# Kernel tuning notes

Hardware: AMD Instinct MI355X
Metric: run time of the kernel (lower is better)

## Reference

```python
import jax, jax.numpy as jnp
import numpy as np

N, E, HID, STRUCT = 50000, 800000, 128, 7
GAMMA, DELTA = 1.0, 0.5
LN_EPS = 1e-5


def seg_softmax(score, seg, num_segments):
    m = jax.ops.segment_max(score, seg, num_segments=num_segments)
    e = jnp.exp(score - m[seg])
    s = jax.ops.segment_sum(e, seg, num_segments=num_segments)
    return e / s[seg]


def setup_inputs() -> dict:
    key = jax.random.key(0)
    ks = jax.random.split(key, 16)
    w = lambda k, shp: (jax.random.normal(k, shp, dtype=jnp.float32) * 0.1)
    return {
        "edge_index": jax.random.randint(ks[0], (2, E), 0, N, dtype=jnp.int32),
        "h": jax.random.normal(ks[1], (N, HID), dtype=jnp.float32),
        "W_att": w(ks[2], (HID, HID)),
        "phi_att_w": w(ks[3], (HID, HID)),
        "phi_att_b": jnp.zeros((HID,), jnp.float32),
        "W_p": w(ks[4], (HID, HID)),
        "W_p_prime": w(ks[5], (HID, HID)),
        "f_def_w": w(ks[6], (HID, 1)),
        "f_def_b": jnp.zeros((1,), jnp.float32),
        "W_self_w": w(ks[7], (HID, HID)),
        "W_self_b": jnp.zeros((HID,), jnp.float32),
        "W_A_w": w(ks[8], (HID, HID)),
        "W_A_b": jnp.zeros((HID,), jnp.float32),
        "W_str_w": w(ks[9], (STRUCT - 1, HID)),
        "W_str_b": jnp.zeros((HID,), jnp.float32),
        "ln_g": jnp.ones((HID,), jnp.float32),
        "ln_b": jnp.zeros((HID,), jnp.float32),
    }


def reference(edge_index, h, W_att, phi_att_w, phi_att_b, W_p, W_p_prime,
              f_def_w, f_def_b, W_self_w, W_self_b, W_A_w, W_A_b,
              W_str_w, W_str_b, ln_g, ln_b):
    H = h  # in_dim == hidden_dim -> embed is None
    s_feat = h[:, : STRUCT - 1]                       # [N, 6]
    src, tgt = edge_index[0], edge_index[1]
    h_src, h_tgt = H[src], H[tgt]                     # [E, HID]
    s_src, s_tgt = s_feat[src], s_feat[tgt]           # [E, 6]

    # attention scores, scatter-softmax over tgt
    W_hs = h_src @ W_att
    score = jnp.sum(h_tgt * W_hs, -1) + jnp.sum(s_src * s_tgt, -1)
    alpha = seg_softmax(score, tgt, N)                # [E]

    # defense term on reversed edges: rev_src = tgt, rev_tgt = src
    h_att, h_def = H[src], H[tgt]                     # H[rev_tgt], H[rev_src]
    pair = jnp.sum((h_att @ W_p) * (h_def @ W_p_prime), -1)
    beta = seg_softmax(pair, src, N)                  # softmax over rev_tgt = src
    psi = (h_def @ f_def_w + f_def_b)[:, 0]           # [E]
    sum_term = jax.ops.segment_sum(beta * jnp.exp(-psi), src, num_segments=N)
    d = -jnp.log(sum_term + 1e-8)
    rho = jax.nn.sigmoid(GAMMA * (d - DELTA))         # [N]

    rho_edge = rho[src]
    m_e = alpha[:, None] * (h_src @ phi_att_w + phi_att_b) * (1.0 - rho_edge)[:, None]
    m_att = jax.ops.segment_sum(m_e, tgt, num_segments=N)  # [N, HID]

    H_new = jax.nn.relu(H @ W_self_w + W_self_b + m_att @ W_A_w + W_A_b
                        + s_feat @ W_str_w + W_str_b) + H
    mu = jnp.mean(H_new, -1, keepdims=True)
    var = jnp.mean((H_new - mu) ** 2, -1, keepdims=True)
    return (H_new - mu) * jax.lax.rsqrt(var + LN_EPS) * ln_g + ln_b
```

## Files before the change

kernel.cpp:

```cpp
#include <hip/hip_runtime.h>
#include <math.h>

#define HID 128
#define NSTR 6
#define GAMMA 1.0f
#define DELTA 0.5f
#define LN_EPS 1e-5f
#define KPAD 72
#define CSR_CHUNK 8192

typedef __attribute__((ext_vector_type(4))) float f4;
typedef __attribute__((ext_vector_type(8))) short bf16x8;
typedef __attribute__((ext_vector_type(4))) float f32x4;

__device__ __forceinline__ unsigned short f2bf(float f) {
    unsigned u = __float_as_uint(f);
    unsigned r = u + 0x7FFFu + ((u >> 16) & 1u);
    return (unsigned short)(r >> 16);
}
__device__ __forceinline__ float bf2f(unsigned short h) {
    return __uint_as_float((unsigned)h << 16);
}
__device__ __forceinline__ void split2(float v, unsigned short& h, unsigned short& l) {
    h = f2bf(v);
    l = f2bf(v - bf2f(h));
}
__device__ __forceinline__ void bf2f2(unsigned u, float& lo, float& hi) {
    lo = __uint_as_float(u << 16);
    hi = __uint_as_float(u & 0xFFFF0000u);
}
__device__ __forceinline__ void unpack8(const uint4 u, float* f) {
    bf2f2(u.x, f[0], f[1]); bf2f2(u.y, f[2], f[3]);
    bf2f2(u.z, f[4], f[5]); bf2f2(u.w, f[6], f[7]);
}

__global__ __launch_bounds__(256) void k_prep_all(
    const float* __restrict__ W_att, const float* __restrict__ Wself,
    const float* __restrict__ Wp,    const float* __restrict__ Wpp,
    const float* __restrict__ phiw,  const float* __restrict__ WA,
    const float* __restrict__ phib,
    unsigned short* __restrict__ WT, float* __restrict__ pbA)
{
    __shared__ float Bs[128][129];
    __shared__ float As[16][129];
    const int mode = blockIdx.y, c0 = blockIdx.x * 16;
    const int tid = threadIdx.x;
    const size_t MSZ = (size_t)2 * HID * HID;
    unsigned short* hi = WT + (size_t)mode * MSZ;
    unsigned short* lo = hi + HID * HID;

    if (mode == 0) {
        for (int idx = tid; idx < 2048; idx += 256) {
            const int c = idx >> 7, k = idx & 127;
            unsigned short h, l;
            split2(W_att[(size_t)(c0 + c) * HID + k], h, l);
            hi[(size_t)(c0 + c) * HID + k] = h;
            lo[(size_t)(c0 + c) * HID + k] = l;
        }
    } else if (mode == 1) {
        for (int idx = tid; idx < 2048; idx += 256) {
            const int k = idx >> 4, c = idx & 15;
            Bs[k][c] = Wself[k * HID + c0 + c];
        }
        __syncthreads();
        for (int idx = tid; idx < 2048; idx += 256) {
            const int c = idx >> 7, k = idx & 127;
            unsigned short h, l;
            split2(Bs[k][c], h, l);
            hi[(size_t)(c0 + c) * HID + k] = h;
            lo[(size_t)(c0 + c) * HID + k] = l;
        }
    } else if (mode == 2) {
        for (int idx = tid; idx < 128 * 128; idx += 256)
            Bs[idx >> 7][idx & 127] = Wpp[idx];
        for (int idx = tid; idx < 16 * 128; idx += 256)
            As[idx >> 7][idx & 127] = Wp[(size_t)(c0 + (idx >> 7)) * HID + (idx & 127)];
        __syncthreads();
        for (int it = 0; it < 8; ++it) {
            const int idx = tid + 256 * it;
            const int c = idx >> 7, k = idx & 127;
            float a = 0.f;
            #pragma unroll 4
            for (int j = 0; j < 128; ++j)
                a = fmaf(As[c][j], Bs[k][j], a);
            unsigned short h, l;
            split2(a, h, l);
            hi[(size_t)(c0 + c) * HID + k] = h;
            lo[(size_t)(c0 + c) * HID + k] = l;
        }
    } else {
        for (int idx = tid; idx < 128 * 128; idx += 256)
            Bs[idx >> 7][idx & 127] = phiw[idx];
        for (int idx = tid; idx < 16 * 128; idx += 256) {
            const int c = idx >> 7, j = idx & 127;
            As[c][j] = WA[(size_t)j * HID + c0 + c];
        }
        __syncthreads();
        for (int it = 0; it < 8; ++it) {
            const int idx = tid + 256 * it;
            const int c = idx >> 7, k = idx & 127;
            float a = 0.f;
            #pragma unroll 4
            for (int j = 0; j < 128; ++j)
                a = fmaf(As[c][j], Bs[k][j], a);
            unsigned short h, l;
            split2(a, h, l);
            hi[(size_t)(c0 + c) * HID + k] = h;
            lo[(size_t)(c0 + c) * HID + k] = l;
        }
        if (tid < 16) {
            float a = 0.f;
            #pragma unroll 4
            for (int j = 0; j < 128; ++j)
                a = fmaf(phib[j], As[tid][j], a);
            pbA[c0 + tid] = a;
        }
    }
}

__global__ __launch_bounds__(256) void k_castpsi(
    const float* __restrict__ H, const float* __restrict__ fw,
    const float* __restrict__ fb,
    unsigned short* __restrict__ HB, float* __restrict__ psi, int N)
{
    const int tid = threadIdx.x;
    const int row = blockIdx.x * 16 + (tid >> 4), sub = tid & 15;
    if (row >= N) return;
    const size_t o = (size_t)row * HID + sub * 8;
    const f4 v0 = *(const f4*)&H[o];
    const f4 v1 = *(const f4*)&H[o + 4];
    ushort4 a, b;
    a.x = f2bf(v0[0]); a.y = f2bf(v0[1]); a.z = f2bf(v0[2]); a.w = f2bf(v0[3]);
    b.x = f2bf(v1[0]); b.y = f2bf(v1[1]); b.z = f2bf(v1[2]); b.w = f2bf(v1[3]);
    *(ushort4*)&HB[o] = a;
    *(ushort4*)&HB[o + 4] = b;
    const f4 w0 = *(const f4*)&fw[sub * 8];
    const f4 w1 = *(const f4*)&fw[sub * 8 + 4];
    float s = v0[0]*w0[0] + v0[1]*w0[1] + v0[2]*w0[2] + v0[3]*w0[3]
            + v1[0]*w1[0] + v1[1]*w1[1] + v1[2]*w1[2] + v1[3]*w1[3];
    #pragma unroll
    for (int mk = 1; mk < 16; mk <<= 1) s += __shfl_xor(s, mk);
    if (sub == 0) psi[row] = s + fb[0];
}

struct GemmArgsT {
    const unsigned short* Whi[2];
    const unsigned short* Wlo[2];
    void*                 O[2];
    int                   of32[2];
};

__global__ __launch_bounds__(256, 2) void k_gemm(const float* __restrict__ A,
                                                 GemmArgsT g, int N)
{
    extern __shared__ unsigned short lds[];
    unsigned short* Ahi = lds;
    unsigned short* Alo = lds + 128 * KPAD;
    unsigned short* Bhi = lds + 2 * 128 * KPAD;
    unsigned short* Blo = lds + 3 * 128 * KPAD;
    const int tid  = threadIdx.x;
    const int row0 = blockIdx.x * 128;
    const int nrows = min(128, N - row0);
    const int ph   = blockIdx.y;
    const int w    = tid >> 6, lane = tid & 63;
    const int lrow = lane & 15, kgrp = lane >> 4;

    f32x4 acc[2][8];
    #pragma unroll
    for (int tc = 0; tc < 8; ++tc) {
        acc[0][tc] = f32x4{0.f, 0.f, 0.f, 0.f};
        acc[1][tc] = f32x4{0.f, 0.f, 0.f, 0.f};
    }

    const unsigned short* __restrict__ Wh = g.Whi[ph];
    const unsigned short* __restrict__ Wl = g.Wlo[ph];

    for (int ch = 0; ch < 2; ++ch) {
        __syncthreads();
        #pragma unroll
        for (int it = 0; it < 8; ++it) {
            const int idx = tid + 256 * it;
            const int r = idx >> 4, kq = (idx & 15) * 4;
            f4 v = {0.f, 0.f, 0.f, 0.f};
            if (r < nrows) v = *(const f4*)&A[(size_t)(row0 + r) * HID + ch * 64 + kq];
            ushort4 h, l;
            split2(v[0], h.x, l.x); split2(v[1], h.y, l.y);
            split2(v[2], h.z, l.z); split2(v[3], h.w, l.w);
            *(ushort4*)&Ahi[r * KPAD + kq] = h;
            *(ushort4*)&Alo[r * KPAD + kq] = l;
        }
        #pragma unroll
        for (int it = 0; it < 4; ++it) {
            const int idx = tid + 256 * it;
            const int c = idx >> 3, k8 = (idx & 7) * 8;
            *(uint4*)&Bhi[c * KPAD + k8] = *(const uint4*)&Wh[(size_t)c * HID + ch * 64 + k8];
            *(uint4*)&Blo[c * KPAD + k8] = *(const uint4*)&Wl[(size_t)c * HID + ch * 64 + k8];
        }
        __syncthreads();

        #pragma unroll
        for (int ks = 0; ks < 2; ++ks) {
            const int ko = ks * 32 + kgrp * 8;
            bf16x8 ah[2], al[2], bh[8], bl[8];
            #pragma unroll
            for (int tr = 0; tr < 2; ++tr) {
                const int rr = w * 32 + tr * 16 + lrow;
                ah[tr] = *(const bf16x8*)&Ahi[rr * KPAD + ko];
                al[tr] = *(const bf16x8*)&Alo[rr * KPAD + ko];
            }
            #pragma unroll
            for (int tc = 0; tc < 8; ++tc) {
                const int cc = tc * 16 + lrow;
                bh[tc] = *(const bf16x8*)&Bhi[cc * KPAD + ko];
                bl[tc] = *(const bf16x8*)&Blo[cc * KPAD + ko];
            }
            #pragma unroll
            for (int tr = 0; tr < 2; ++tr)
                #pragma unroll
                for (int tc = 0; tc < 8; ++tc) {
                    acc[tr][tc] = __builtin_amdgcn_mfma_f32_16x16x32_bf16(ah[tr], bh[tc], acc[tr][tc], 0, 0, 0);
                    acc[tr][tc] = __builtin_amdgcn_mfma_f32_16x16x32_bf16(al[tr], bh[tc], acc[tr][tc], 0, 0, 0);
                    acc[tr][tc] = __builtin_amdgcn_mfma_f32_16x16x32_bf16(ah[tr], bl[tc], acc[tr][tc], 0, 0, 0);
                }
        }
    }

    #pragma unroll
    for (int tr = 0; tr < 2; ++tr)
        #pragma unroll
        for (int j = 0; j < 4; ++j) {
            const int r = w * 32 + tr * 16 + kgrp * 4 + j;
            if (r < nrows) {
                if (g.of32[ph]) {
                    float* O = (float*)g.O[ph];
                    #pragma unroll
                    for (int tc = 0; tc < 8; ++tc)
                        O[(size_t)(row0 + r) * HID + tc * 16 + lrow] = acc[tr][tc][j];
                } else {
                    unsigned short* O = (unsigned short*)g.O[ph];
                    #pragma unroll
                    for (int tc = 0; tc < 8; ++tc)
                        O[(size_t)(row0 + r) * HID + tc * 16 + lrow] = f2bf(acc[tr][tc][j]);
                }
            }
        }
}

__global__ __launch_bounds__(256, 2) void k_final(
    const float* __restrict__ Agg, const float* __restrict__ H,
    const float* __restrict__ sig, const float* __restrict__ pbA,
    const unsigned short* __restrict__ Ghi, const unsigned short* __restrict__ Glo,
    const unsigned short* __restrict__ WShi, const unsigned short* __restrict__ WSlo,
    const float* __restrict__ Wstr,
    const float* __restrict__ bself, const float* __restrict__ bA,
    const float* __restrict__ bstr,
    const float* __restrict__ lng, const float* __restrict__ lnb,
    float* __restrict__ out, int N)
{
    extern __shared__ unsigned short lds[];
    unsigned short* Ahi = lds;
    unsigned short* Alo = lds + 128 * KPAD;
    unsigned short* Bhi = lds + 2 * 128 * KPAD;
    unsigned short* Blo = lds + 3 * 128 * KPAD;
    const int tid  = threadIdx.x;
    const int row0 = blockIdx.x * 128;
    const int nrows = min(128, N - row0);
    const int w    = tid >> 6, lane = tid & 63;
    const int lrow = lane & 15, kgrp = lane >> 4;

    f32x4 acc[2][8];
    float gl[8], bl_[8], pb[8];
    #pragma unroll
    for (int tc = 0; tc < 8; ++tc) {
        const int c = tc * 16 + lrow;
        const float bv = bself[c] + bA[c] + bstr[c];
        acc[0][tc] = f32x4{bv, bv, bv, bv};
        acc[1][tc] = f32x4{bv, bv, bv, bv};
        gl[tc] = lng[c]; bl_[tc] = lnb[c]; pb[tc] = pbA[c];
    }

    for (int ph = 0; ph < 2; ++ph) {
        const float* __restrict__ Am = ph ? H : Agg;
        const unsigned short* __restrict__ Wh = ph ? WShi : Ghi;
        const unsigned short* __restrict__ Wl = ph ? WSlo : Glo;
        for (int ch = 0; ch < 2; ++ch) {
            __syncthreads();
            #pragma unroll
            for (int it = 0; it < 8; ++it) {
                const int idx = tid + 256 * it;
                const int r = idx >> 4, kq = (idx & 15) * 4;
                f4 v = {0.f, 0.f, 0.f, 0.f};
                if (r < nrows) v = *(const f4*)&Am[(size_t)(row0 + r) * HID + ch * 64 + kq];
                ushort4 h, l;
                split2(v[0], h.x, l.x); split2(v[1], h.y, l.y);
                split2(v[2], h.z, l.z); split2(v[3], h.w, l.w);
                *(ushort4*)&Ahi[r * KPAD + kq] = h;
                *(ushort4*)&Alo[r * KPAD + kq] = l;
            }
            #pragma unroll
            for (int it = 0; it < 4; ++it) {
                const int idx = tid + 256 * it;
                const int c = idx >> 3, k8 = (idx & 7) * 8;
                *(uint4*)&Bhi[c * KPAD + k8] = *(const uint4*)&Wh[(size_t)c * HID + ch * 64 + k8];
                *(uint4*)&Blo[c * KPAD + k8] = *(const uint4*)&Wl[(size_t)c * HID + ch * 64 + k8];
            }
            __syncthreads();

            #pragma unroll
            for (int ks = 0; ks < 2; ++ks) {
                const int ko = ks * 32 + kgrp * 8;
                bf16x8 ah[2], al[2], bh[8], bl[8];
                #pragma unroll
                for (int tr = 0; tr < 2; ++tr) {
                    const int rr = w * 32 + tr * 16 + lrow;
                    ah[tr] = *(const bf16x8*)&Ahi[rr * KPAD + ko];
                    al[tr] = *(const bf16x8*)&Alo[rr * KPAD + ko];
                }
                #pragma unroll
                for (int tc = 0; tc < 8; ++tc) {
                    const int cc = tc * 16 + lrow;
                    bh[tc] = *(const bf16x8*)&Bhi[cc * KPAD + ko];
                    bl[tc] = *(const bf16x8*)&Blo[cc * KPAD + ko];
                }
                #pragma unroll
                for (int tr = 0; tr < 2; ++tr)
                    #pragma unroll
                    for (int tc = 0; tc < 8; ++tc) {
                        acc[tr][tc] = __builtin_amdgcn_mfma_f32_16x16x32_bf16(ah[tr], bh[tc], acc[tr][tc], 0, 0, 0);
                        acc[tr][tc] = __builtin_amdgcn_mfma_f32_16x16x32_bf16(al[tr], bh[tc], acc[tr][tc], 0, 0, 0);
                        acc[tr][tc] = __builtin_amdgcn_mfma_f32_16x16x32_bf16(ah[tr], bl[tc], acc[tr][tc], 0, 0, 0);
                    }
            }

            if (ph == 1 && ch == 0) {
                #pragma unroll
                for (int tr = 0; tr < 2; ++tr)
                    #pragma unroll
                    for (int j = 0; j < 4; ++j) {
                        const int rr = w * 32 + tr * 16 + kgrp * 4 + j;
                        float s[NSTR];
                        #pragma unroll
                        for (int k = 0; k < NSTR; ++k)
                            s[k] = bf2f(Ahi[rr * KPAD + k]) + bf2f(Alo[rr * KPAD + k]);
                        #pragma unroll
                        for (int tc = 0; tc < 8; ++tc) {
                            float a = 0.f;
                            #pragma unroll
                            for (int k = 0; k < NSTR; ++k)
                                a = fmaf(s[k], Wstr[k * HID + tc * 16 + lrow], a);
                            acc[tr][tc][j] += a;
                        }
                    }
            }
        }
    }

    #pragma unroll
    for (int tr = 0; tr < 2; ++tr)
        #pragma unroll
        for (int j = 0; j < 4; ++j) {
            const int r = w * 32 + tr * 16 + kgrp * 4 + j;
            const bool valid = r < nrows;
            const size_t rb = (size_t)(row0 + r) * HID;
            const float sg = valid ? sig[row0 + r] : 0.f;
            float v[8], s1 = 0.f, s2 = 0.f;
            #pragma unroll
            for (int tc = 0; tc < 8; ++tc) {
                float x = fmaxf(acc[tr][tc][j] + sg * pb[tc], 0.f);
                if (valid) x += H[rb + tc * 16 + lrow];
                v[tc] = x;
                s1 += x; s2 += x * x;
            }
            #pragma unroll
            for (int mk = 1; mk < 16; mk <<= 1) {
                s1 += __shfl_xor(s1, mk);
                s2 += __shfl_xor(s2, mk);
            }
            const float mean = s1 * (1.f / HID);
            const float var  = s2 * (1.f / HID) - mean * mean;
            const float rs   = rsqrtf(var + LN_EPS);
            if (valid) {
                #pragma unroll
                for (int tc = 0; tc < 8; ++tc)
                    out[rb + tc * 16 + lrow] = (v[tc] - mean) * rs * gl[tc] + bl_[tc];
            }
        }
}

__global__ __launch_bounds__(256) void k_csr_count(
    const int* __restrict__ etgt, const int* __restrict__ esrc,
    int* __restrict__ cnt_t, int* __restrict__ cnt_s,
    int NB, int NC, int E)
{
    __shared__ int cnt[256];
    const int which = blockIdx.y;
    const int* __restrict__ key = which ? esrc : etgt;
    int* __restrict__ outc = which ? cnt_s : cnt_t;
    const int tid = threadIdx.x;
    for (int i = tid; i < NB; i += 256) cnt[i] = 0;
    __syncthreads();
    const int e0 = blockIdx.x * CSR_CHUNK;
    const int e1 = min(e0 + CSR_CHUNK, E);
    for (int e = e0 + tid; e < e1; e += 256)
        atomicAdd(&cnt[key[e] >> 8], 1);
    __syncthreads();
    for (int k = tid; k < NB; k += 256)
        outc[(size_t)k * NC + blockIdx.x] = cnt[k];
}

__global__ __launch_bounds__(1024) void k_csr_scan(
    const int* __restrict__ cnt_t, int* __restrict__ off_t,
    const int* __restrict__ cnt_s, int* __restrict__ off_s, int L)
{
    const int* __restrict__ cnt = blockIdx.x ? cnt_s : cnt_t;
    int* __restrict__ off = blockIdx.x ? off_s : off_t;
    __shared__ int warp_sums[16];
    __shared__ int carry_s;
    const int tid = threadIdx.x, lane = tid & 63, wid = tid >> 6;
    if (tid == 0) carry_s = 0;
    __syncthreads();
    for (int i0 = 0; i0 < L; i0 += 1024) {
        const int i = i0 + tid;
        const int v = (i < L) ? cnt[i] : 0;
        int x = v;
        #pragma unroll
        for (int d = 1; d < 64; d <<= 1) {
            const int y = __shfl_up(x, d);
            if (lane >= d) x += y;
        }
        if (lane == 63) warp_sums[wid] = x;
        __syncthreads();
        if (wid == 0) {
            int ws = (lane < 16) ? warp_sums[lane] : 0;
            #pragma unroll
            for (int d = 1; d < 16; d <<= 1) {
                const int y = __shfl_up(ws, d);
                if (lane >= d) ws += y;
            }
            if (lane < 16) warp_sums[lane] = ws;
        }
        __syncthreads();
        const int carry = carry_s;
        if (i < L) off[i] = carry + (wid ? warp_sums[wid - 1] : 0) + x - v;
        __syncthreads();
        if (tid == 1023) carry_s = carry + warp_sums[15];
        __syncthreads();
    }
    if (tid == 0) off[L] = carry_s;
}

__global__ __launch_bounds__(256) void k_csr_bucket(
    const int* __restrict__ etgt, const int* __restrict__ esrc,
    const int* __restrict__ off_t, const int* __restrict__ off_s,
    int* __restrict__ ebuck_t, int* __restrict__ ebuck_s,
    int NB, int NC, int E)
{
    __shared__ int cur[256];
    const int which = blockIdx.y;
    const int* __restrict__ key = which ? esrc : etgt;
    const int* __restrict__ off = which ? off_s : off_t;
    int* __restrict__ ebuck = which ? ebuck_s : ebuck_t;
    const int tid = threadIdx.x;
    for (int k = tid; k < NB; k += 256)
        cur[k] = off[(size_t)k * NC + blockIdx.x];
    __syncthreads();
    const int e0 = blockIdx.x * CSR_CHUNK;
    const int e1 = min(e0 + CSR_CHUNK, E);
    for (int e = e0 + tid; e < e1; e += 256) {
        const int p = atomicAdd(&cur[key[e] >> 8], 1);
        ebuck[p] = e;
    }
}

__global__ __launch_bounds__(256) void k_csr_final(
    const int* __restrict__ etgt, const int* __restrict__ esrc,
    const int* __restrict__ off_t, const int* __restrict__ off_s,
    const int* __restrict__ ebuck_t, const int* __restrict__ ebuck_s,
    int* __restrict__ base_t, int* __restrict__ base_s,
    int* __restrict__ eid_t, int* __restrict__ eid_s,
    int* __restrict__ src_t, int* __restrict__ tgt_s,
    int NB, int NC, int N, int E)
{
    __shared__ int cnt[256], excl[256], wsum[4];
    const int which = blockIdx.y;
    const int* __restrict__ key   = which ? esrc : etgt;
    const int* __restrict__ oth   = which ? etgt : esrc;
    const int* __restrict__ off   = which ? off_s : off_t;
    const int* __restrict__ ebuck = which ? ebuck_s : ebuck_t;
    int* __restrict__ base = which ? base_s : base_t;
    int* __restrict__ eid  = which ? eid_s : eid_t;
    int* __restrict__ aux  = which ? tgt_s : src_t;
    const int tid = threadIdx.x, lane = tid & 63, wv = tid >> 6;
    const int k = blockIdx.x;
    const int segb = off[(size_t)k * NC];
    const int sege = (k + 1 < NB) ? off[(size_t)(k + 1) * NC] : E;
    cnt[tid] = 0;
    __syncthreads();
    for (int i = segb + tid; i < sege; i += 256)
        atomicAdd(&cnt[key[ebuck[i]] & 255], 1);
    __syncthreads();
    {
        const int orig = cnt[tid];
        int x = orig;
        #pragma unroll
        for (int d = 1; d < 64; d <<= 1) {
            const int y = __shfl_up(x, d);
            if (lane >= d) x += y;
        }
        if (lane == 63) wsum[wv] = x;
        __syncthreads();
        if (tid == 0) {
            int a = 0;
            #pragma unroll
            for (int i = 0; i < 4; ++i) { const int t = wsum[i]; wsum[i] = a; a += t; }
        }
        __syncthreads();
        excl[tid] = x - orig + wsum[wv];
    }
    __syncthreads();
    const int node = k * 256 + tid;
    if (node < N) base[node] = segb + excl[tid];
    if (k == NB - 1 && tid == 0) base[N] = E;
    cnt[tid] = excl[tid];
    __syncthreads();
    for (int i = segb + tid; i < sege; i += 256) {
        const int e = ebuck[i];
        const int r = atomicAdd(&cnt[key[e] & 255], 1);
        eid[segb + r] = e;
        aux[segb + r] = oth[e];
    }
}

__global__ __launch_bounds__(256) void k_score(
    const int* __restrict__ eid_t, const int* __restrict__ base_t,
    const int* __restrict__ src_t,
    const float* __restrict__ Wt, const unsigned short* __restrict__ UB,
    const unsigned short* __restrict__ HB,
    float* __restrict__ score, float* __restrict__ pairv,
    float* __restrict__ sumt_inv, int N)
{
    const int lane = threadIdx.x & 63, wv = threadIdx.x >> 6;
    const int t = blockIdx.x * 4 + wv;
    if (t >= N) return;
    const int b0 = base_t[t], deg = base_t[t + 1] - b0;
    if (deg == 0) { if (lane == 0) sumt_inv[t] = 0.f; return; }
    const int sub = lane & 15, grp = lane >> 4;
    const size_t to = (size_t)t * HID;

    float wt[8], u[8], htg[8];
    {
        const f4 w0 = *(const f4*)&Wt[to + sub * 8];
        const f4 w1 = *(const f4*)&Wt[to + sub * 8 + 4];
        wt[0] = w0[0]; wt[1] = w0[1]; wt[2] = w0[2]; wt[3] = w0[3];
        wt[4] = w1[0]; wt[5] = w1[1]; wt[6] = w1[2]; wt[7] = w1[3];
        unpack8(*(const uint4*)&UB[to + sub * 8], u);
        unpack8(*(const uint4*)&HB[to + sub * 8], htg);
    }

    bool valN = grp < deg;
    int eidN = 0, srcN = 0;
    if (valN) { eidN = eid_t[b0 + grp]; srcN = src_t[b0 + grp]; }

    for (int j0 = 0; j0 < deg; j0 += 4) {
        const bool val = valN;
        const int eid = eidN, src = srcN;
        const uint4 raw = *(const uint4*)&HB[(size_t)src * HID + sub * 8];
        const int jn = j0 + 4 + grp;
        valN = jn < deg;
        eidN = 0; srcN = 0;
        if (valN) { eidN = eid_t[b0 + jn]; srcN = src_t[b0 + jn]; }

        float hs[8];
        unpack8(raw, hs);
        float ps = 0.f, pp = 0.f;
        #pragma unroll
        for (int d = 0; d < 8; ++d) {
            ps = fmaf(wt[d], hs[d], ps);
            pp = fmaf(u[d], hs[d], pp);
        }
        if (sub == 0) {
            #pragma unroll
            for (int d = 0; d < NSTR; ++d) ps = fmaf(htg[d], hs[d], ps);
        }
        #pragma unroll
        for (int mk = 1; mk < 16; mk <<= 1) {
            ps += __shfl_xor(ps, mk);
            pp += __shfl_xor(pp, mk);
        }
        if (sub == 0 && val) {
            score[b0 + j0 + grp] = ps;
            pairv[eid] = pp;
        }
    }

    float m = -1e30f;
    for (int i = lane; i < deg; i += 64) m = fmaxf(m, score[b0 + i]);
    #pragma unroll
    for (int mk = 1; mk < 64; mk <<= 1) m = fmaxf(m, __shfl_xor(m, mk));
    float psum = 0.f;
    for (int i = lane; i < deg; i += 64) {
        const float e = expf(score[b0 + i] - m);
        score[b0 + i] = e;
        psum += e;
    }
    #pragma unroll
    for (int mk = 1; mk < 64; mk <<= 1) psum += __shfl_xor(psum, mk);
    if (lane == 0) sumt_inv[t] = 1.f / psum;
}

__global__ __launch_bounds__(256) void k_beta2(
    const int* __restrict__ base_s, const int* __restrict__ eid_s,
    const int* __restrict__ tgt_s,
    const float* __restrict__ pairv, const float* __restrict__ psi,
    float* __restrict__ rho1m, int N)
{
    const int lane = threadIdx.x & 63, wv = threadIdx.x >> 6;
    const int s = blockIdx.x * 4 + wv;
    if (s >= N) return;
    const int b0 = base_s[s], deg = base_s[s + 1] - b0;

    float m = -1e30f;
    for (int i = lane; i < deg; i += 64) m = fmaxf(m, pairv[eid_s[b0 + i]]);
    #pragma unroll
    for (int mk = 1; mk < 64; mk <<= 1) m = fmaxf(m, __shfl_xor(m, mk));

    float se = 0.f, sn = 0.f;
    for (int i = lane; i < deg; i += 64) {
        const float ex = expf(pairv[eid_s[b0 + i]] - m);
        se += ex;
        sn += ex * expf(-psi[tgt_s[b0 + i]]);
    }
    #pragma unroll
    for (int mk = 1; mk < 64; mk <<= 1) {
        se += __shfl_xor(se, mk);
        sn += __shfl_xor(sn, mk);
    }
    if (lane == 0) {
        const float st = (deg > 0 && se > 0.f) ? sn / se : 0.f;
        const float d  = -logf(st + 1e-8f);
        rho1m[s] = 1.f - 1.f / (1.f + expf(-(GAMMA * (d - DELTA))));
    }
}

__global__ __launch_bounds__(256) void k_matt(
    const int* __restrict__ src_t, const int* __restrict__ base_t,
    const float* __restrict__ score, const float* __restrict__ sumt_inv,
    const float* __restrict__ rho1m,
    const unsigned short* __restrict__ HB,
    float* __restrict__ agg, float* __restrict__ sig, int N)
{
    const int lane = threadIdx.x & 63, wv = threadIdx.x >> 6;
    const int t = blockIdx.x * 4 + wv;
    if (t >= N) return;
    const int b0 = base_t[t], deg = base_t[t + 1] - b0;
    const int sub = lane & 15, grp = lane >> 4;
    const size_t to = (size_t)t * HID;

    float acc[8];
    #pragma unroll
    for (int d = 0; d < 8; ++d) acc[d] = 0.f;
    float csum = 0.f;
    const float inv = (deg > 0) ? sumt_inv[t] : 0.f;

    for (int j0 = 0; j0 < deg; j0 += 8) {
        const int jA = j0 + grp, jB = j0 + 4 + grp;
        const bool vA = jA < deg, vB = jB < deg;
        float cA = 0.f, cB = 0.f;
        size_t soA = 0, soB = 0;
        if (vA) {
            const int s = src_t[b0 + jA];
            cA = score[b0 + jA] * inv * rho1m[s];
            soA = (size_t)s * HID;
        }
        if (vB) {
            const int s = src_t[b0 + jB];
            cB = score[b0 + jB] * inv * rho1m[s];
            soB = (size_t)s * HID;
        }
        const uint4 rA = *(const uint4*)&HB[soA + sub * 8];
        const uint4 rB = *(const uint4*)&HB[soB + sub * 8];
        float hA[8], hB[8];
        unpack8(rA, hA); unpack8(rB, hB);
        #pragma unroll
        for (int d = 0; d < 8; ++d) {
            acc[d] = fmaf(cA, hA[d], acc[d]);
            acc[d] = fmaf(cB, hB[d], acc[d]);
        }
        if (sub == 0) csum += cA + cB;
    }
    #pragma unroll
    for (int d = 0; d < 8; ++d) {
        acc[d] += __shfl_xor(acc[d], 16);
        acc[d] += __shfl_xor(acc[d], 32);
    }
    csum += __shfl_xor(csum, 16);
    csum += __shfl_xor(csum, 32);
    if (grp == 0) {
        f4 o0, o1;
        #pragma unroll
        for (int d = 0; d < 4; ++d) { o0[d] = acc[d]; o1[d] = acc[d + 4]; }
        *(f4*)&agg[to + sub * 8]     = o0;
        *(f4*)&agg[to + sub * 8 + 4] = o1;
        if (sub == 0) sig[t] = csum;
    }
}

extern "C" void kernel_launch(void* const* d_in, const int* in_sizes, int n_in,
                              void* d_out, int out_size, void* d_ws, size_t ws_size,
                              hipStream_t stream)
{
    const int*   eidx   = (const int*)  d_in[0];
    const float* H      = (const float*)d_in[1];
    const float* W_att  = (const float*)d_in[2];
    const float* phi_w  = (const float*)d_in[3];
    const float* phi_b  = (const float*)d_in[4];
    const float* W_p    = (const float*)d_in[5];
    const float* W_pp   = (const float*)d_in[6];
    const float* fdef_w = (const float*)d_in[7];
    const float* fdef_b = (const float*)d_in[8];
    const float* Wself  = (const float*)d_in[9];
    const float* bself  = (const float*)d_in[10];
    const float* WA     = (const float*)d_in[11];
    const float* bA     = (const float*)d_in[12];
    const float* Wstr   = (const float*)d_in[13];
    const float* bstr   = (const float*)d_in[14];
    const float* lng    = (const float*)d_in[15];
    const float* lnb    = (const float*)d_in[16];
    float* out = (float*)d_out;

    const int E = in_sizes[0] / 2;
    const int N = in_sizes[1] / HID;
    const int* esrc = eidx;
    const int* etgt = eidx + E;

    const int NB = (N + 255) >> 8;
    const int NC = (E + CSR_CHUNK - 1) / CSR_CHUNK;
    const int L  = NB * NC;

    char* w = (char*)d_ws;
    const size_t NHb  = (size_t)N * HID * sizeof(unsigned short);
    const size_t NH   = (size_t)N * HID * sizeof(float);
    const size_t Epad = (((size_t)E * sizeof(float)) + 255) & ~255ull;
    const size_t Npad = (((size_t)(N + 1) * sizeof(float)) + 255) & ~255ull;
    const size_t Lpad = (((size_t)(L + 1) * sizeof(int)) + 255) & ~255ull;

    float*          Wt    = (float*)w;          w += NH;
    unsigned short* UB    = (unsigned short*)w; w += NHb;
    unsigned short* HB    = (unsigned short*)w; w += NHb;
    float* score   = (float*)w; w += Epad;
    float* pairv   = (float*)w; w += Epad;
    int*   eid_t   = (int*)  w; w += Epad;
    int*   eid_s   = (int*)  w; w += Epad;
    int*   src_t   = (int*)  w; w += Epad;
    int*   tgt_s   = (int*)  w; w += Epad;
    int*   ebuck_t = (int*)  w; w += Epad;
    int*   ebuck_s = (int*)  w; w += Epad;
    int*   cnt_t = (int*)w; w += Lpad;
    int*   off_t = (int*)w; w += Lpad;
    int*   cnt_s = (int*)w; w += Lpad;
    int*   off_s = (int*)w; w += Lpad;
    int*   base_t   = (int*)  w; w += Npad;
    int*   base_s   = (int*)  w; w += Npad;
    float* sumt_inv = (float*)w; w += Npad;
    float* psi      = (float*)w; w += Npad;
    float* rho1m    = (float*)w; w += Npad;
    float* sig      = (float*)w; w += Npad;
    float* pbA      = (float*)w; w += 512;
    unsigned short* WT = (unsigned short*)w;
    w += 4 * 2 * HID * HID * sizeof(unsigned short);
    float* agg = Wt;

    const int nblk128 = (N + 127) / 128;
    const int nblkN4  = (N + 3) / 4;
    const size_t lds_mfma = 4 * 128 * KPAD * sizeof(unsigned short);
    const size_t MSZ = (size_t)2 * HID * HID;

    k_prep_all<<<dim3(8, 4), 256, 0, stream>>>(W_att, Wself, W_p, W_pp,
                                               phi_w, WA, phi_b, WT, pbA);

    k_castpsi<<<(N + 15) / 16, 256, 0, stream>>>(H, fdef_w, fdef_b, HB, psi, N);

    GemmArgsT g2;
    g2.Whi[0] = WT;           g2.Wlo[0] = WT + HID * HID;
    g2.Whi[1] = WT + 2 * MSZ; g2.Wlo[1] = WT + 2 * MSZ + HID * HID;
    g2.O[0] = Wt;  g2.of32[0] = 1;
    g2.O[1] = UB;  g2.of32[1] = 0;
    k_gemm<<<dim3(nblk128, 2), 256, lds_mfma, stream>>>(H, g2, N);

    k_csr_count<<<dim3(NC, 2), 256, 0, stream>>>(etgt, esrc, cnt_t, cnt_s, NB, NC, E);
    k_csr_scan<<<2, 1024, 0, stream>>>(cnt_t, off_t, cnt_s, off_s, L);
    k_csr_bucket<<<dim3(NC, 2), 256, 0, stream>>>(etgt, esrc, off_t, off_s,
                                                  ebuck_t, ebuck_s, NB, NC, E);
    k_csr_final<<<dim3(NB, 2), 256, 0, stream>>>(etgt, esrc, off_t, off_s,
                                                 ebuck_t, ebuck_s, base_t, base_s,
                                                 eid_t, eid_s, src_t, tgt_s,
                                                 NB, NC, N, E);

    k_score<<<nblkN4, 256, 0, stream>>>(eid_t, base_t, src_t, Wt, UB, HB,
                                        score, pairv, sumt_inv, N);
    k_beta2<<<nblkN4, 256, 0, stream>>>(base_s, eid_s, tgt_s, pairv, psi, rho1m, N);

    k_matt<<<nblkN4, 256, 0, stream>>>(src_t, base_t, score, sumt_inv,
                                       rho1m, HB, agg, sig, N);

    k_final<<<nblk128, 256, lds_mfma, stream>>>(agg, H, sig, pbA,
                                                WT + 3 * MSZ, WT + 3 * MSZ + HID * HID,
                                                WT + 1 * MSZ, WT + 1 * MSZ + HID * HID,
                                                Wstr, bself, bA, bstr, lng, lnb, out, N);
}
```

Baseline: 305.3 us.

## Fuse cast/psi with CSR count, single-pass beta for small degree, prefetch in matt

The bf16 cast/psi kernel and the CSR histogram count kernel are merged into one launch, with block ranges split by role. This removes a launch and lets the two independent jobs run at the same time. k_beta2 gets a single-pass path for degree at most 64 that avoids reloading pairv through eid_s. k_matt software-prefetches the next group's source indices and scores, so index loads overlap with the gather of HB rows.

```diff
diff --git a/kernel.cpp b/kernel.cpp
--- a/kernel.cpp
+++ b/kernel.cpp
@@ -118,29 +118,50 @@
     }
 }
 
-__global__ __launch_bounds__(256) void k_castpsi(
+__global__ __launch_bounds__(256) void k_cast_count(
     const float* __restrict__ H, const float* __restrict__ fw,
     const float* __restrict__ fb,
-    unsigned short* __restrict__ HB, float* __restrict__ psi, int N)
-{
+    unsigned short* __restrict__ HB, float* __restrict__ psi,
+    const int* __restrict__ etgt, const int* __restrict__ esrc,
+    int* __restrict__ cnt_t, int* __restrict__ cnt_s,
+    int nbCast, int NB, int NC, int E, int N)
+{
+    __shared__ int cnt[256];
     const int tid = threadIdx.x;
-    const int row = blockIdx.x * 16 + (tid >> 4), sub = tid & 15;
-    if (row >= N) return;
-    const size_t o = (size_t)row * HID + sub * 8;
-    const f4 v0 = *(const f4*)&H[o];
-    const f4 v1 = *(const f4*)&H[o + 4];
-    ushort4 a, b;
-    a.x = f2bf(v0[0]); a.y = f2bf(v0[1]); a.z = f2bf(v0[2]); a.w = f2bf(v0[3]);
-    b.x = f2bf(v1[0]); b.y = f2bf(v1[1]); b.z = f2bf(v1[2]); b.w = f2bf(v1[3]);
-    *(ushort4*)&HB[o] = a;
-    *(ushort4*)&HB[o + 4] = b;
-    const f4 w0 = *(const f4*)&fw[sub * 8];
-    const f4 w1 = *(const f4*)&fw[sub * 8 + 4];
-    float s = v0[0]*w0[0] + v0[1]*w0[1] + v0[2]*w0[2] + v0[3]*w0[3]
-            + v1[0]*w1[0] + v1[1]*w1[1] + v1[2]*w1[2] + v1[3]*w1[3];
-    #pragma unroll
-    for (int mk = 1; mk < 16; mk <<= 1) s += __shfl_xor(s, mk);
-    if (sub == 0) psi[row] = s + fb[0];
+    const int bid = blockIdx.x;
+    if (bid < nbCast) {
+        const int row = bid * 16 + (tid >> 4), sub = tid & 15;
+        if (row >= N) return;
+        const size_t o = (size_t)row * HID + sub * 8;
+        const f4 v0 = *(const f4*)&H[o];
+        const f4 v1 = *(const f4*)&H[o + 4];
+        ushort4 a, b;
+        a.x = f2bf(v0[0]); a.y = f2bf(v0[1]); a.z = f2bf(v0[2]); a.w = f2bf(v0[3]);
+        b.x = f2bf(v1[0]); b.y = f2bf(v1[1]); b.z = f2bf(v1[2]); b.w = f2bf(v1[3]);
+        *(ushort4*)&HB[o] = a;
+        *(ushort4*)&HB[o + 4] = b;
+        const f4 w0 = *(const f4*)&fw[sub * 8];
+        const f4 w1 = *(const f4*)&fw[sub * 8 + 4];
+        float s = v0[0]*w0[0] + v0[1]*w0[1] + v0[2]*w0[2] + v0[3]*w0[3]
+                + v1[0]*w1[0] + v1[1]*w1[1] + v1[2]*w1[2] + v1[3]*w1[3];
+        #pragma unroll
+        for (int mk = 1; mk < 16; mk <<= 1) s += __shfl_xor(s, mk);
+        if (sub == 0) psi[row] = s + fb[0];
+    } else {
+        const int rem = bid - nbCast;
+        const int which = rem / NC, blk = rem % NC;
+        const int* __restrict__ key = which ? esrc : etgt;
+        int* __restrict__ outc = which ? cnt_s : cnt_t;
+        for (int i = tid; i < NB; i += 256) cnt[i] = 0;
+        __syncthreads();
+        const int e0 = blk * CSR_CHUNK;
+        const int e1 = min(e0 + CSR_CHUNK, E);
+        for (int e = e0 + tid; e < e1; e += 256)
+            atomicAdd(&cnt[key[e] >> 8], 1);
+        __syncthreads();
+        for (int k = tid; k < NB; k += 256)
+            outc[(size_t)k * NC + blk] = cnt[k];
+    }
 }
 
 struct GemmArgsT {
@@ -387,27 +408,6 @@
         }
 }
 
-__global__ __launch_bounds__(256) void k_csr_count(
-    const int* __restrict__ etgt, const int* __restrict__ esrc,
-    int* __restrict__ cnt_t, int* __restrict__ cnt_s,
-    int NB, int NC, int E)
-{
-    __shared__ int cnt[256];
-    const int which = blockIdx.y;
-    const int* __restrict__ key = which ? esrc : etgt;
-    int* __restrict__ outc = which ? cnt_s : cnt_t;
-    const int tid = threadIdx.x;
-    for (int i = tid; i < NB; i += 256) cnt[i] = 0;
-    __syncthreads();
-    const int e0 = blockIdx.x * CSR_CHUNK;
-    const int e1 = min(e0 + CSR_CHUNK, E);
-    for (int e = e0 + tid; e < e1; e += 256)
-        atomicAdd(&cnt[key[e] >> 8], 1);
-    __syncthreads();
-    for (int k = tid; k < NB; k += 256)
-        outc[(size_t)k * NC + blockIdx.x] = cnt[k];
-}
-
 __global__ __launch_bounds__(1024) void k_csr_scan(
     const int* __restrict__ cnt_t, int* __restrict__ off_t,
     const int* __restrict__ cnt_s, int* __restrict__ off_s, int L)
@@ -619,16 +619,28 @@
     if (s >= N) return;
     const int b0 = base_s[s], deg = base_s[s + 1] - b0;
 
-    float m = -1e30f;
-    for (int i = lane; i < deg; i += 64) m = fmaxf(m, pairv[eid_s[b0 + i]]);
-    #pragma unroll
-    for (int mk = 1; mk < 64; mk <<= 1) m = fmaxf(m, __shfl_xor(m, mk));
-
     float se = 0.f, sn = 0.f;
-    for (int i = lane; i < deg; i += 64) {
-        const float ex = expf(pairv[eid_s[b0 + i]] - m);
-        se += ex;
-        sn += ex * expf(-psi[tgt_s[b0 + i]]);
+    if (deg <= 64) {
+        const bool v = lane < deg;
+        float pv = -1e30f;
+        int tg = 0;
+        if (v) { pv = pairv[eid_s[b0 + lane]]; tg = tgt_s[b0 + lane]; }
+        float m = pv;
+        #pragma unroll
+        for (int mk = 1; mk < 64; mk <<= 1) m = fmaxf(m, __shfl_xor(m, mk));
+        const float ex = v ? expf(pv - m) : 0.f;
+        se = ex;
+        sn = v ? ex * expf(-psi[tg]) : 0.f;
+    } else {
+        float m = -1e30f;
+        for (int i = lane; i < deg; i += 64) m = fmaxf(m, pairv[eid_s[b0 + i]]);
+        #pragma unroll
+        for (int mk = 1; mk < 64; mk <<= 1) m = fmaxf(m, __shfl_xor(m, mk));
+        for (int i = lane; i < deg; i += 64) {
+            const float ex = expf(pairv[eid_s[b0 + i]] - m);
+            se += ex;
+            sn += ex * expf(-psi[tgt_s[b0 + i]]);
+        }
     }
     #pragma unroll
     for (int mk = 1; mk < 64; mk <<= 1) {
@@ -662,23 +674,28 @@
     float csum = 0.f;
     const float inv = (deg > 0) ? sumt_inv[t] : 0.f;
 
+    bool vA = grp < deg, vB = 4 + grp < deg;
+    int sA = 0, sB = 0;
+    float scA = 0.f, scB = 0.f;
+    if (vA) { sA = src_t[b0 + grp];     scA = score[b0 + grp]; }
+    if (vB) { sB = src_t[b0 + 4 + grp]; scB = score[b0 + 4 + grp]; }
+
     for (int j0 = 0; j0 < deg; j0 += 8) {
-        const int jA = j0 + grp, jB = j0 + 4 + grp;
-        const bool vA = jA < deg, vB = jB < deg;
-        float cA = 0.f, cB = 0.f;
-        size_t soA = 0, soB = 0;
-        if (vA) {
-            const int s = src_t[b0 + jA];
-            cA = score[b0 + jA] * inv * rho1m[s];
-            soA = (size_t)s * HID;
-        }
-        if (vB) {
-            const int s = src_t[b0 + jB];
-            cB = score[b0 + jB] * inv * rho1m[s];
-            soB = (size_t)s * HID;
-        }
-        const uint4 rA = *(const uint4*)&HB[soA + sub * 8];
-        const uint4 rB = *(const uint4*)&HB[soB + sub * 8];
+        const bool cvA = vA, cvB = vB;
+        const int csA = sA, csB = sB;
+        const float cscA = scA, cscB = scB;
+        const float rhoA = cvA ? rho1m[csA] : 0.f;
+        const float rhoB = cvB ? rho1m[csB] : 0.f;
+        const uint4 rA = *(const uint4*)&HB[(size_t)csA * HID + sub * 8];
+        const uint4 rB = *(const uint4*)&HB[(size_t)csB * HID + sub * 8];
+        const int jA = j0 + 8 + grp, jB = j0 + 12 + grp;
+        vA = jA < deg; vB = jB < deg;
+        sA = sB = 0; scA = scB = 0.f;
+        if (vA) { sA = src_t[b0 + jA]; scA = score[b0 + jA]; }
+        if (vB) { sB = src_t[b0 + jB]; scB = score[b0 + jB]; }
+
+        const float cA = cvA ? cscA * inv * rhoA : 0.f;
+        const float cB = cvB ? cscB * inv * rhoB : 0.f;
         float hA[8], hB[8];
         unpack8(rA, hA); unpack8(rB, hB);
         #pragma unroll
@@ -772,13 +789,16 @@
 
     const int nblk128 = (N + 127) / 128;
     const int nblkN4  = (N + 3) / 4;
+    const int nbCast  = (N + 15) / 16;
     const size_t lds_mfma = 4 * 128 * KPAD * sizeof(unsigned short);
     const size_t MSZ = (size_t)2 * HID * HID;
 
     k_prep_all<<<dim3(8, 4), 256, 0, stream>>>(W_att, Wself, W_p, W_pp,
                                                phi_w, WA, phi_b, WT, pbA);
 
-    k_castpsi<<<(N + 15) / 16, 256, 0, stream>>>(H, fdef_w, fdef_b, HB, psi, N);
+    k_cast_count<<<nbCast + 2 * NC, 256, 0, stream>>>(H, fdef_w, fdef_b, HB, psi,
+                                                      etgt, esrc, cnt_t, cnt_s,
+                                                      nbCast, NB, NC, E, N);
 
     GemmArgsT g2;
     g2.Whi[0] = WT;           g2.Wlo[0] = WT + HID * HID;
@@ -787,7 +807,6 @@
     g2.O[1] = UB;  g2.of32[1] = 0;
     k_gemm<<<dim3(nblk128, 2), 256, lds_mfma, stream>>>(H, g2, N);
 
-    k_csr_count<<<dim3(NC, 2), 256, 0, stream>>>(etgt, esrc, cnt_t, cnt_s, NB, NC, E);
     k_csr_scan<<<2, 1024, 0, stream>>>(cnt_t, off_t, cnt_s, off_s, L);
     k_csr_bucket<<<dim3(NC, 2), 256, 0, stream>>>(etgt, esrc, off_t, off_s,
                                                   ebuck_t, ebuck_s, NB, NC, E);
```

Result: faster. 294.0 us (-3.7%).
